# Optimization experiments

Hardware: AMD Instinct MI355X
Metric: run time of the kernel (lower is better)

The kernel has to match this reference:

```python
import jax, jax.numpy as jnp
import numpy as np

BATCH, SEQ, HIDDEN = 4096, 200, 64


def setup_inputs() -> dict:
    key = jax.random.key(0)
    ks = jax.random.split(key, 7)
    s = 1.0 / np.sqrt(HIDDEN)  # torch LSTM default init scale
    return {
        "inputs": jax.random.normal(ks[0], (BATCH, SEQ, 1), dtype=jnp.float32),
        "W_ih": jax.random.uniform(ks[1], (4 * HIDDEN, 1), jnp.float32, -s, s),
        "W_hh": jax.random.uniform(ks[2], (4 * HIDDEN, HIDDEN), jnp.float32, -s, s),
        "b_ih": jax.random.uniform(ks[3], (4 * HIDDEN,), jnp.float32, -s, s),
        "b_hh": jax.random.uniform(ks[4], (4 * HIDDEN,), jnp.float32, -s, s),
        "W_lin": jax.random.uniform(ks[5], (1, SEQ * HIDDEN), jnp.float32, -s, s),
        "b_lin": jax.random.uniform(ks[6], (1,), jnp.float32, -s, s),
    }


def _lstm(inputs, W_ih, W_hh, b_ih, b_hh):
    # inputs: [B, T, 1] (batch_first). Precompute input projections for all t.
    B, T, _ = inputs.shape
    H = W_hh.shape[1]
    # [T, B, 4H]
    x_proj = jnp.einsum('bti,gi->tbg', inputs, W_ih) + (b_ih + b_hh)

    def step(carry, xg):
        h, c = carry
        gates = xg + h @ W_hh.T  # [B, 4H]
        i, f, g, o = jnp.split(gates, 4, axis=-1)
        i = jax.nn.sigmoid(i)
        f = jax.nn.sigmoid(f)
        g = jnp.tanh(g)
        o = jax.nn.sigmoid(o)
        c = f * c + i * g
        h = o * jnp.tanh(c)
        return (h, c), h

    h0 = jnp.zeros((B, H), dtype=inputs.dtype)
    c0 = jnp.zeros((B, H), dtype=inputs.dtype)
    _, hs = jax.lax.scan(step, (h0, c0), x_proj)  # hs: [T, B, H]
    return jnp.transpose(hs, (1, 0, 2))  # [B, T, H]


def reference(inputs, W_ih, W_hh, b_ih, b_hh, W_lin, b_lin):
    hs = _lstm(inputs, W_ih, W_hh, b_ih, b_hh)          # [B, T, H]
    flat = hs.reshape(hs.shape[0], -1)                   # [B, T*H]
    return flat @ W_lin.T + b_lin                        # [B, 1]
```

## Files before the change

### kernel.cpp

```cpp
#include <hip/hip_runtime.h>

#define SEQ 200
#define HID 64
#define BT  8
#define NBLK (4096 / BT)

typedef _Float16 f16;
typedef _Float16 f16x8 __attribute__((ext_vector_type(8)));
typedef float    f32x4 __attribute__((ext_vector_type(4)));

#define LOG2E 1.44269504088896340736f

#if __has_builtin(__builtin_amdgcn_exp2f)
#define EXP2F(x) __builtin_amdgcn_exp2f(x)
#else
#define EXP2F(x) __expf(0.69314718056f * (x))
#endif
#define RCPF(x) __builtin_amdgcn_rcpf(x)

__device__ __forceinline__ float sigmoid_s(float s) {
    return RCPF(1.0f + EXP2F(-s));
}
__device__ __forceinline__ float tanh_s2(float s2) {
    return fmaf(-2.0f, RCPF(1.0f + EXP2F(s2)), 1.0f);
}

__global__ __launch_bounds__(256, 2)
void qlstm_v12(const float* __restrict__ x,
               const float* __restrict__ W_ih,
               const float* __restrict__ W_hh,
               const float* __restrict__ b_ih,
               const float* __restrict__ b_hh,
               const float* __restrict__ W_lin,
               const float* __restrict__ b_lin,
               float* __restrict__ out)
{
    __shared__ float x_lds[BT][201];
    __shared__ f16   h_frag[2][16 * HID];
    __shared__ float wl_lds[SEQ * HID];
    __shared__ float out_part[4][BT];

    const int tid = threadIdx.x;
    const int w   = tid >> 6;
    const int l   = tid & 63;
    const int m   = l & 15;
    const int a   = l >> 4;
    const int b0  = blockIdx.x * BT;

    const float qs[4] = {LOG2E, LOG2E, 2.0f * LOG2E, LOG2E};

    for (int i = tid; i < BT * SEQ; i += 256) {
        int b = i / SEQ, t = i - b * SEQ;
        x_lds[b][t] = x[(size_t)b0 * SEQ + i];
    }
    {
        const float4* src = (const float4*)W_lin;
        float4* dst = (float4*)wl_lds;
        for (int i = tid; i < SEQ * HID / 4; i += 256) dst[i] = src[i];
    }
    for (int i = tid; i < 1024; i += 256) ((float*)h_frag)[i] = 0.0f;

    f16x8 Bf[4][2];
    float wihq[4], biasq[4];
    #pragma unroll
    for (int q = 0; q < 4; ++q) {
        const int n = q * 64 + w * 16 + m;
        wihq[q]  = W_ih[n] * qs[q];
        biasq[q] = (b_ih[n] + b_hh[n]) * qs[q];
        #pragma unroll
        for (int kk = 0; kk < 2; ++kk) {
            const float4* p = (const float4*)(W_hh + n * HID + kk * 32 + a * 8);
            float4 lo = p[0], hi = p[1];
            f16x8 f;
            f[0] = (f16)(lo.x * qs[q]); f[1] = (f16)(lo.y * qs[q]);
            f[2] = (f16)(lo.z * qs[q]); f[3] = (f16)(lo.w * qs[q]);
            f[4] = (f16)(hi.x * qs[q]); f[5] = (f16)(hi.y * qs[q]);
            f[6] = (f16)(hi.z * qs[q]); f[7] = (f16)(hi.w * qs[q]);
            Bf[q][kk] = f;
        }
    }

    const int jpw = w * 16 + m;
    const int ra0 = m * 128 + (((0 + a) ^ (m & 7)) << 4);
    const int ra1 = m * 128 + (((4 + a) ^ (m & 7)) << 4);
    const int bA = 2 * a;
    const int bB = 2 * a + 1;
    int hwr[4];
    #pragma unroll
    for (int r = 0; r < 4; ++r) {
        const int R = 4 * a + r;
        hwr[r] = R * 128 + ((((jpw >> 3) ^ (R & 7))) << 4) + (jpw & 7) * 2;
    }

    const char* hbytes = (const char*)h_frag;

    float cA = 0.0f, cB = 0.0f, oA = 0.0f, oB = 0.0f;
    const float t2s = 2.0f * LOG2E;

    __syncthreads();

    for (int t = 0; t < SEQ; ++t) {
        const int rb = (t & 1) << 11;
        const int wb = rb ^ 2048;

        __builtin_amdgcn_s_setprio(1);
        const f16x8 A0 = *(const f16x8*)(hbytes + rb + ra0);
        const f16x8 A1 = *(const f16x8*)(hbytes + rb + ra1);
        const float x0 = x_lds[bA][t];
        const float x1 = x_lds[bB][t];
        const float wl = wl_lds[t * HID + jpw];

        f32x4 acc[4];
        #pragma unroll
        for (int q = 0; q < 4; ++q) {
            const float i0 = fmaf(x0, wihq[q], biasq[q]);
            const float i1 = fmaf(x1, wihq[q], biasq[q]);
            f32x4 ini;
            ini[0] = i0; ini[1] = i1; ini[2] = i0; ini[3] = i1;
            f32x4 z = __builtin_amdgcn_mfma_f32_16x16x32_f16(A0, Bf[q][0], ini, 0, 0, 0);
            acc[q]  = __builtin_amdgcn_mfma_f32_16x16x32_f16(A1, Bf[q][1], z, 0, 0, 0);
        }
        __builtin_amdgcn_s_setprio(0);

        {
            const float gi = sigmoid_s(acc[0][0]);
            const float gf = sigmoid_s(acc[1][0]);
            const float gg = tanh_s2(acc[2][0]);
            const float go = sigmoid_s(acc[3][0]);
            cA = fmaf(gf, cA, t2s * (gi * gg));
            const float h = go * tanh_s2(cA);
            const f16 hf = (f16)h;
            *(f16*)((char*)h_frag + wb + hwr[0]) = hf;
            *(f16*)((char*)h_frag + wb + hwr[2]) = hf;
            oA = fmaf(h, wl, oA);
        }
        {
            const float gi = sigmoid_s(acc[0][1]);
            const float gf = sigmoid_s(acc[1][1]);
            const float gg = tanh_s2(acc[2][1]);
            const float go = sigmoid_s(acc[3][1]);
            cB = fmaf(gf, cB, t2s * (gi * gg));
            const float h = go * tanh_s2(cB);
            const f16 hf = (f16)h;
            *(f16*)((char*)h_frag + wb + hwr[1]) = hf;
            *(f16*)((char*)h_frag + wb + hwr[3]) = hf;
            oB = fmaf(h, wl, oB);
        }

        __syncthreads();
    }

    float vA = oA, vB = oB;
    #pragma unroll
    for (int off = 1; off < 16; off <<= 1) {
        vA += __shfl_xor(vA, off, 64);
        vB += __shfl_xor(vB, off, 64);
    }
    if (m == 0) {
        out_part[w][bA] = vA;
        out_part[w][bB] = vB;
    }
    __syncthreads();
    if (tid < BT) {
        out[b0 + tid] = out_part[0][tid] + out_part[1][tid]
                      + out_part[2][tid] + out_part[3][tid] + b_lin[0];
    }
}

extern "C" void kernel_launch(void* const* d_in, const int* in_sizes, int n_in,
                              void* d_out, int out_size, void* d_ws, size_t ws_size,
                              hipStream_t stream) {
    const float* x     = (const float*)d_in[0];
    const float* W_ih  = (const float*)d_in[1];
    const float* W_hh  = (const float*)d_in[2];
    const float* b_ih  = (const float*)d_in[3];
    const float* b_hh  = (const float*)d_in[4];
    const float* W_lin = (const float*)d_in[5];
    const float* b_lin = (const float*)d_in[6];
    float* out = (float*)d_out;

    dim3 grid(NBLK);
    dim3 block(256);
    qlstm_v12<<<grid, block, 0, stream>>>(x, W_ih, W_hh, b_ih, b_hh,
                                          W_lin, b_lin, out);
}
```

Baseline: 94.78 us.

## Halve per-block batch tile and read output weights from global memory

Each block now handles 4 batch rows instead of 8, so every MFMA row carries one batch element replicated four times instead of two. The 51KB W_lin shared buffer is dropped and each step reads W_lin directly from global/L2 memory. This cuts shared memory use and allows 4 blocks per CU, which raises occupancy and doubles the grid, so more latency on the serial recurrence can be hidden. The cost is half the MFMA utilization per block (twice the total MFMA work) and a global load on every timestep.

```diff
diff --git a/kernel.cpp b/kernel.cpp
--- a/kernel.cpp
+++ b/kernel.cpp
@@ -2,7 +2,7 @@
 
 #define SEQ 200
 #define HID 64
-#define BT  8
+#define BT  4
 #define NBLK (4096 / BT)
 
 typedef _Float16 f16;
@@ -25,8 +25,8 @@
     return fmaf(-2.0f, RCPF(1.0f + EXP2F(s2)), 1.0f);
 }
 
-__global__ __launch_bounds__(256, 2)
-void qlstm_v12(const float* __restrict__ x,
+__global__ __launch_bounds__(256, 4)
+void qlstm_v13(const float* __restrict__ x,
                const float* __restrict__ W_ih,
                const float* __restrict__ W_hh,
                const float* __restrict__ b_ih,
@@ -37,7 +37,6 @@
 {
     __shared__ float x_lds[BT][201];
     __shared__ f16   h_frag[2][16 * HID];
-    __shared__ float wl_lds[SEQ * HID];
     __shared__ float out_part[4][BT];
 
     const int tid = threadIdx.x;
@@ -52,11 +51,6 @@
     for (int i = tid; i < BT * SEQ; i += 256) {
         int b = i / SEQ, t = i - b * SEQ;
         x_lds[b][t] = x[(size_t)b0 * SEQ + i];
-    }
-    {
-        const float4* src = (const float4*)W_lin;
-        float4* dst = (float4*)wl_lds;
-        for (int i = tid; i < SEQ * HID / 4; i += 256) dst[i] = src[i];
     }
     for (int i = tid; i < 1024; i += 256) ((float*)h_frag)[i] = 0.0f;
 
@@ -83,18 +77,16 @@
     const int jpw = w * 16 + m;
     const int ra0 = m * 128 + (((0 + a) ^ (m & 7)) << 4);
     const int ra1 = m * 128 + (((4 + a) ^ (m & 7)) << 4);
-    const int bA = 2 * a;
-    const int bB = 2 * a + 1;
     int hwr[4];
     #pragma unroll
     for (int r = 0; r < 4; ++r) {
         const int R = 4 * a + r;
-        hwr[r] = R * 128 + ((((jpw >> 3) ^ (R & 7))) << 4) + (jpw & 7) * 2;
+        hwr[r] = R * 128 + (((jpw >> 3) ^ (R & 7)) << 4) + (jpw & 7) * 2;
     }
 
     const char* hbytes = (const char*)h_frag;
 
-    float cA = 0.0f, cB = 0.0f, oA = 0.0f, oB = 0.0f;
+    float c = 0.0f, o = 0.0f;
     const float t2s = 2.0f * LOG2E;
 
     __syncthreads();
@@ -103,63 +95,45 @@
         const int rb = (t & 1) << 11;
         const int wb = rb ^ 2048;
 
+        const float wl = W_lin[t * HID + jpw];
+
         __builtin_amdgcn_s_setprio(1);
         const f16x8 A0 = *(const f16x8*)(hbytes + rb + ra0);
         const f16x8 A1 = *(const f16x8*)(hbytes + rb + ra1);
-        const float x0 = x_lds[bA][t];
-        const float x1 = x_lds[bB][t];
-        const float wl = wl_lds[t * HID + jpw];
+        const float xv = x_lds[a][t];
 
         f32x4 acc[4];
         #pragma unroll
         for (int q = 0; q < 4; ++q) {
-            const float i0 = fmaf(x0, wihq[q], biasq[q]);
-            const float i1 = fmaf(x1, wihq[q], biasq[q]);
+            const float i0 = fmaf(xv, wihq[q], biasq[q]);
             f32x4 ini;
-            ini[0] = i0; ini[1] = i1; ini[2] = i0; ini[3] = i1;
+            ini[0] = i0; ini[1] = i0; ini[2] = i0; ini[3] = i0;
             f32x4 z = __builtin_amdgcn_mfma_f32_16x16x32_f16(A0, Bf[q][0], ini, 0, 0, 0);
             acc[q]  = __builtin_amdgcn_mfma_f32_16x16x32_f16(A1, Bf[q][1], z, 0, 0, 0);
         }
         __builtin_amdgcn_s_setprio(0);
 
-        {
-            const float gi = sigmoid_s(acc[0][0]);
-            const float gf = sigmoid_s(acc[1][0]);
-            const float gg = tanh_s2(acc[2][0]);
-            const float go = sigmoid_s(acc[3][0]);
-            cA = fmaf(gf, cA, t2s * (gi * gg));
-            const float h = go * tanh_s2(cA);
-            const f16 hf = (f16)h;
-            *(f16*)((char*)h_frag + wb + hwr[0]) = hf;
-            *(f16*)((char*)h_frag + wb + hwr[2]) = hf;
-            oA = fmaf(h, wl, oA);
-        }
-        {
-            const float gi = sigmoid_s(acc[0][1]);
-            const float gf = sigmoid_s(acc[1][1]);
-            const float gg = tanh_s2(acc[2][1]);
-            const float go = sigmoid_s(acc[3][1]);
-            cB = fmaf(gf, cB, t2s * (gi * gg));
-            const float h = go * tanh_s2(cB);
-            const f16 hf = (f16)h;
-            *(f16*)((char*)h_frag + wb + hwr[1]) = hf;
-            *(f16*)((char*)h_frag + wb + hwr[3]) = hf;
-            oB = fmaf(h, wl, oB);
-        }
+        const float gi = sigmoid_s(acc[0][0]);
+        const float gf = sigmoid_s(acc[1][0]);
+        const float gg = tanh_s2(acc[2][0]);
+        const float go = sigmoid_s(acc[3][0]);
+        c = fmaf(gf, c, t2s * (gi * gg));
+        const float h = go * tanh_s2(c);
+        const f16 hf = (f16)h;
+        *(f16*)((char*)h_frag + wb + hwr[0]) = hf;
+        *(f16*)((char*)h_frag + wb + hwr[1]) = hf;
+        *(f16*)((char*)h_frag + wb + hwr[2]) = hf;
+        *(f16*)((char*)h_frag + wb + hwr[3]) = hf;
+        o = fmaf(h, wl, o);
 
         __syncthreads();
     }
 
-    float vA = oA, vB = oB;
+    float v = o;
     #pragma unroll
-    for (int off = 1; off < 16; off <<= 1) {
-        vA += __shfl_xor(vA, off, 64);
-        vB += __shfl_xor(vB, off, 64);
-    }
-    if (m == 0) {
-        out_part[w][bA] = vA;
-        out_part[w][bB] = vB;
-    }
+    for (int off = 1; off < 16; off <<= 1)
+        v += __shfl_xor(v, off, 64);
+    if (m == 0) out_part[w][a] = v;
     __syncthreads();
     if (tid < BT) {
         out[b0 + tid] = out_part[0][tid] + out_part[1][tid]
@@ -181,6 +155,6 @@
 
     dim3 grid(NBLK);
     dim3 block(256);
-    qlstm_v12<<<grid, block, 0, stream>>>(x, W_ih, W_hh, b_ih, b_hh,
+    qlstm_v13<<<grid, block, 0, stream>>>(x, W_ih, W_hh, b_ih, b_hh,
                                           W_lin, b_lin, out);
 }
```

Result: slower. 133.4 us (+40.8%).
